# Kernel tuning notes

Measured on AMD Instinct MI355X. Metric: run time of the kernel, lower is better.

## Reference

```python
import jax, jax.numpy as jnp
import numpy as np

N = 100000        # nodes
E = 1600000       # directed edges (avg degree 16)
F_IN, F_HID, F_OUT = 512, 32, 16


def setup_inputs() -> dict:
    key = jax.random.key(0)
    k0, k1, k2, k3 = jax.random.split(key, 4)
    x = jax.random.normal(k0, (N, F_IN), dtype=jnp.float32)
    edge_index = jax.random.randint(k1, (2, E), 0, N, dtype=jnp.int32)
    # Glorot-ish init for the two GCNConv linear weights
    W1 = jax.random.normal(k2, (F_IN, F_HID), dtype=jnp.float32) / np.float32(np.sqrt(F_IN))
    W2 = jax.random.normal(k3, (F_HID, F_OUT), dtype=jnp.float32) / np.float32(np.sqrt(F_HID))
    b1 = jnp.zeros((F_HID,), jnp.float32)
    b2 = jnp.zeros((F_OUT,), jnp.float32)
    return {"x": x, "W1": W1, "b1": b1, "W2": W2, "b2": b2, "edge_index": edge_index}


def gcn_conv(x, W, b, src, dst):
    """PyG GCNConv: h = x W; symmetric-normalized aggregation with self-loops; + bias."""
    h = x @ W                                   # [N, F_out] project first (PyG order)
    # degree including the implicit self-loop (start from ones)
    deg = jnp.ones((N,), h.dtype).at[dst].add(1.0)
    dinv = jax.lax.rsqrt(deg)                   # deg^{-1/2}
    coef = (dinv[src] * dinv[dst])[:, None]     # [E, 1] edge norm
    msg = h[src] * coef                         # gather + scale
    agg = jax.ops.segment_sum(msg, dst, num_segments=N)  # scatter-add to dst
    agg = agg + h * (dinv * dinv)[:, None]      # self-loop contribution
    return agg + b


def reference(x, W1, b1, W2, b2, edge_index):
    src, dst = edge_index[0], edge_index[1]
    h = jax.nn.relu(gcn_conv(x, W1, b1, src, dst))
    # F.dropout(training=self.training) is identity in eval mode
    h = gcn_conv(h, W2, b2, src, dst)
    return jax.nn.log_softmax(h, axis=1)
```

## Files before the change

kernel.cpp:

```cpp
#include <hip/hip_runtime.h>
#include <hip/hip_bf16.h>
#include <cstdint>

#define NN   100000
#define NE   1600000
#define FIN  512
#define FHID 32
#define FOUT 16

#define BSHIFT 9
#define BSIZE  512
#define NBUCK  196
#define EPB    4096
#define NCHUNK ((NE + EPB - 1) / EPB)

typedef float f32x4 __attribute__((ext_vector_type(4)));
typedef short s16x8 __attribute__((ext_vector_type(8)));
typedef short s16x4 __attribute__((ext_vector_type(4)));
typedef unsigned int u32;
typedef unsigned short u16;

__device__ __forceinline__ short f2bf(float f) {
  union { float f; uint32_t u; } v; v.f = f;
  uint32_t r = v.u + 0x7fffu + ((v.u >> 16) & 1u);
  return (short)(r >> 16);
}
__device__ __forceinline__ float bf2f(u16 u) {
  union { uint32_t u; float f; } v; v.u = (uint32_t)u << 16; return v.f;
}

__global__ __launch_bounds__(256) void k_hist(const int* __restrict__ dst,
                                              u32* __restrict__ bcount) {
  __shared__ u32 h[NBUCK];
  int tid = threadIdx.x;
  if (tid < NBUCK) h[tid] = 0;
  __syncthreads();
  int base = blockIdx.x * EPB;
  #pragma unroll
  for (int i = 0; i < EPB / 256; ++i) {
    int e = base + i * 256 + tid;
    if (e < NE) atomicAdd(&h[dst[e] >> BSHIFT], 1u);
  }
  __syncthreads();
  if (tid < NBUCK && h[tid]) atomicAdd(&bcount[tid], h[tid]);
}

__global__ __launch_bounds__(256) void k_bscan(const u32* __restrict__ bc,
                                               u32* __restrict__ bstart,
                                               u32* __restrict__ bcur) {
  __shared__ u32 tmp[256];
  int tid = threadIdx.x;
  u32 v = (tid < NBUCK) ? bc[tid] : 0;
  tmp[tid] = v;
  __syncthreads();
  #pragma unroll
  for (int off = 1; off < 256; off <<= 1) {
    u32 t = (tid >= off) ? tmp[tid - off] : 0;
    __syncthreads();
    tmp[tid] += t;
    __syncthreads();
  }
  if (tid < NBUCK) { u32 e = tmp[tid] - v; bstart[tid] = e; bcur[tid] = e; }
  if (tid == 255) bstart[NBUCK] = tmp[255];
}

__global__ __launch_bounds__(256) void k_bin(const int* __restrict__ src,
                                             const int* __restrict__ dst,
                                             u32* __restrict__ bcur,
                                             u32* __restrict__ binned) {
  __shared__ u32 cnt[NBUCK];
  __shared__ u32 lofs[NBUCK];
  __shared__ u32 gbase[NBUCK];
  __shared__ u32 tmp[256];
  __shared__ u32 stage[EPB];
  __shared__ u16 sb[EPB];
  int tid = threadIdx.x;
  if (tid < NBUCK) cnt[tid] = 0;
  __syncthreads();

  int base = blockIdx.x * EPB;
  u32 vals[EPB / 256];
  u32 ofs[EPB / 256];
  int bks[EPB / 256];
  #pragma unroll
  for (int i = 0; i < EPB / 256; ++i) {
    int e = base + i * 256 + tid;
    bool ok = e < NE;
    int s = 0, d = 0;
    if (ok) { s = src[e]; d = dst[e]; }
    int b = ok ? (d >> BSHIFT) : -1;
    bks[i] = b;
    vals[i] = (u32)s | ((u32)(d & (BSIZE - 1)) << 17);
    ofs[i] = ok ? atomicAdd(&cnt[b], 1u) : 0;
  }
  __syncthreads();

  u32 cv = (tid < NBUCK) ? cnt[tid] : 0;
  tmp[tid] = cv;
  __syncthreads();
  #pragma unroll
  for (int off = 1; off < 256; off <<= 1) {
    u32 t = (tid >= off) ? tmp[tid - off] : 0;
    __syncthreads();
    tmp[tid] += t;
    __syncthreads();
  }
  if (tid < NBUCK) {
    lofs[tid] = tmp[tid] - cv;
    gbase[tid] = cv ? atomicAdd(&bcur[tid], cv) : 0;
  }
  __syncthreads();
  u32 total = tmp[255];
  __syncthreads();

  #pragma unroll
  for (int i = 0; i < EPB / 256; ++i) {
    if (bks[i] >= 0) {
      u32 sl = lofs[bks[i]] + ofs[i];
      stage[sl] = vals[i];
      sb[sl] = (u16)bks[i];
    }
  }
  __syncthreads();

  for (u32 s2 = tid; s2 < total; s2 += 256) {
    int b = sb[s2];
    binned[gbase[b] + (s2 - lofs[b])] = stage[s2];
  }
}

__global__ __launch_bounds__(256) void k_fin(const u32* __restrict__ binned,
                                             const u32* __restrict__ bstart,
                                             int* __restrict__ deg,
                                             int* __restrict__ rs,
                                             float* __restrict__ dinv,
                                             int* __restrict__ csr) {
  __shared__ u32 degl[BSIZE];
  __shared__ u32 rsl[BSIZE];
  __shared__ u32 tmp[256];
  int tid = threadIdx.x;
  int b = blockIdx.x;
  u32 start = bstart[b];
  u32 n = bstart[b + 1] - start;

  degl[tid] = 0; degl[tid + 256] = 0;
  __syncthreads();
  for (u32 k = tid; k < n; k += 256)
    atomicAdd(&degl[binned[start + k] >> 17], 1u);
  __syncthreads();

  u32 a0 = degl[2 * tid], a1 = degl[2 * tid + 1];
  u32 s = a0 + a1;
  tmp[tid] = s;
  __syncthreads();
  #pragma unroll
  for (int off = 1; off < 256; off <<= 1) {
    u32 t = (tid >= off) ? tmp[tid - off] : 0;
    __syncthreads();
    tmp[tid] += t;
    __syncthreads();
  }
  u32 e = tmp[tid] - s;
  rsl[2 * tid] = e;
  rsl[2 * tid + 1] = e + a0;
  __syncthreads();

  #pragma unroll
  for (int q = 0; q < 2; ++q) {
    int t = tid + q * 256;
    int g = b * BSIZE + t;
    if (g < NN) {
      deg[g] = (int)degl[t];
      rs[g] = (int)(start + rsl[t]);
      dinv[g] = rsqrtf(1.0f + (float)degl[t]);
    }
  }
  __syncthreads();

  for (u32 k = tid; k < n; k += 256) {
    u32 v = binned[start + k];
    u32 pos = atomicAdd(&rsl[v >> 17], 1u);
    csr[start + pos] = (int)(v & 0x1FFFFu);
  }
}

__global__ __launch_bounds__(256) void k_gemm1(const float* __restrict__ x,
                                               const float* __restrict__ W1,
                                               const float* __restrict__ dinv,
                                               u16* __restrict__ Hs1) {
  __shared__ s16x8 Blds[16][2][64];
  const int tid = threadIdx.x;
  for (int it = 0; it < 64; ++it) {
    int flat = it * 256 + tid;
    int i  = flat & 7;
    int l  = (flat >> 3) & 63;
    int nt = (flat >> 9) & 1;
    int kt = flat >> 10;
    int k  = kt * 32 + ((l >> 4) << 3) + i;
    int n  = nt * 16 + (l & 15);
    ((short*)Blds)[flat] = f2bf(W1[k * 32 + n]);
  }
  __syncthreads();

  const int lane = tid & 63;
  const int wv   = tid >> 6;
  const int h    = lane >> 4;
  const int m    = lane & 15;
  const int wid  = blockIdx.x * 4 + wv;
  if (wid >= 3125) return;
  const int t0 = wid * 2;

  const float* xr0 = x + (size_t)(t0 * 16 + m) * FIN + h * 8;
  const float* xr1 = xr0 + (size_t)16 * FIN;

  f32x4 acc[2][2] = {};
  #pragma unroll
  for (int kt = 0; kt < 16; ++kt) {
    f32x4 a0 = *(const f32x4*)(xr0 + kt * 32);
    f32x4 a1 = *(const f32x4*)(xr0 + kt * 32 + 4);
    f32x4 c0 = *(const f32x4*)(xr1 + kt * 32);
    f32x4 c1 = *(const f32x4*)(xr1 + kt * 32 + 4);
    s16x8 b0 = Blds[kt][0][lane];
    s16x8 b1 = Blds[kt][1][lane];
    s16x8 af, cf;
    af[0]=f2bf(a0[0]); af[1]=f2bf(a0[1]); af[2]=f2bf(a0[2]); af[3]=f2bf(a0[3]);
    af[4]=f2bf(a1[0]); af[5]=f2bf(a1[1]); af[6]=f2bf(a1[2]); af[7]=f2bf(a1[3]);
    cf[0]=f2bf(c0[0]); cf[1]=f2bf(c0[1]); cf[2]=f2bf(c0[2]); cf[3]=f2bf(c0[3]);
    cf[4]=f2bf(c1[0]); cf[5]=f2bf(c1[1]); cf[6]=f2bf(c1[2]); cf[7]=f2bf(c1[3]);
    acc[0][0] = __builtin_amdgcn_mfma_f32_16x16x32_bf16(af, b0, acc[0][0], 0, 0, 0);
    acc[0][1] = __builtin_amdgcn_mfma_f32_16x16x32_bf16(af, b1, acc[0][1], 0, 0, 0);
    acc[1][0] = __builtin_amdgcn_mfma_f32_16x16x32_bf16(cf, b0, acc[1][0], 0, 0, 0);
    acc[1][1] = __builtin_amdgcn_mfma_f32_16x16x32_bf16(cf, b1, acc[1][1], 0, 0, 0);
  }
  #pragma unroll
  for (int rt = 0; rt < 2; ++rt) {
    #pragma unroll
    for (int r = 0; r < 4; ++r) {
      int row = (t0 + rt) * 16 + h * 4 + r;
      float di = dinv[row];
      u16* o = Hs1 + (size_t)row * FHID + m;
      o[0]  = (u16)f2bf(acc[rt][0][r] * di);
      o[16] = (u16)f2bf(acc[rt][1][r] * di);
    }
  }
}

__global__ __launch_bounds__(256) void k_gat1(const int* __restrict__ csr,
                                              const int* __restrict__ rs,
                                              const int* __restrict__ deg,
                                              const float* __restrict__ dinv,
                                              const float* __restrict__ b1,
                                              const float* __restrict__ W2,
                                              const u16* __restrict__ Hs1,
                                              u16* __restrict__ Hs2) {
  __shared__ float w[FHID * FOUT];
  for (int i = threadIdx.x; i < FHID * FOUT; i += 256) w[i] = W2[i];
  __syncthreads();

  int t = blockIdx.x * 256 + threadIdx.x;
  int d = t >> 2;
  if (d >= NN) return;
  int p = t & 3;
  int start = rs[d], n = deg[d];

  float a0[8], a1[8], a2[8], a3[8];
  {
    s16x8 v = *(const s16x8*)(Hs1 + (size_t)d * FHID + p * 8);
    #pragma unroll
    for (int k = 0; k < 8; ++k) {
      a0[k] = bf2f((u16)v[k]); a1[k] = 0.f; a2[k] = 0.f; a3[k] = 0.f;
    }
  }
  int j = 0;
  for (; j + 4 <= n; j += 4) {
    int s0 = csr[start + j];
    int s1 = csr[start + j + 1];
    int s2 = csr[start + j + 2];
    int s3 = csr[start + j + 3];
    s16x8 v0 = *(const s16x8*)(Hs1 + (size_t)s0 * FHID + p * 8);
    s16x8 v1 = *(const s16x8*)(Hs1 + (size_t)s1 * FHID + p * 8);
    s16x8 v2 = *(const s16x8*)(Hs1 + (size_t)s2 * FHID + p * 8);
    s16x8 v3 = *(const s16x8*)(Hs1 + (size_t)s3 * FHID + p * 8);
    #pragma unroll
    for (int k = 0; k < 8; ++k) {
      a0[k] += bf2f((u16)v0[k]);
      a1[k] += bf2f((u16)v1[k]);
      a2[k] += bf2f((u16)v2[k]);
      a3[k] += bf2f((u16)v3[k]);
    }
  }
  for (; j < n; ++j) {
    int s0 = csr[start + j];
    s16x8 v0 = *(const s16x8*)(Hs1 + (size_t)s0 * FHID + p * 8);
    #pragma unroll
    for (int k = 0; k < 8; ++k) a0[k] += bf2f((u16)v0[k]);
  }

  float dd = dinv[d];
  float h[8];
  #pragma unroll
  for (int k = 0; k < 8; ++k)
    h[k] = fmaxf(((a0[k] + a1[k]) + (a2[k] + a3[k])) * dd + b1[p * 8 + k], 0.0f);

  float pj[FOUT];
  #pragma unroll
  for (int jj = 0; jj < FOUT; ++jj) pj[jj] = 0.f;
  #pragma unroll
  for (int k = 0; k < 8; ++k)
    #pragma unroll
    for (int jj = 0; jj < FOUT; ++jj)
      pj[jj] = fmaf(h[k], w[(p * 8 + k) * FOUT + jj], pj[jj]);
  #pragma unroll
  for (int jj = 0; jj < FOUT; ++jj) {
    pj[jj] += __shfl_xor(pj[jj], 1);
    pj[jj] += __shfl_xor(pj[jj], 2);
  }
  s16x4 o;
  #pragma unroll
  for (int q = 0; q < 4; ++q) o[q] = f2bf(pj[p * 4 + q] * dd);
  *(s16x4*)(Hs2 + (size_t)d * FOUT + p * 4) = o;
}

__global__ __launch_bounds__(256) void k_gat2(const int* __restrict__ csr,
                                              const int* __restrict__ rs,
                                              const int* __restrict__ deg,
                                              const float* __restrict__ dinv,
                                              const float* __restrict__ b2,
                                              const u16* __restrict__ Hs2,
                                              float* __restrict__ out) {
  int t = blockIdx.x * 256 + threadIdx.x;
  int d = t >> 1;
  if (d >= NN) return;
  int p = t & 1;
  int start = rs[d], n = deg[d];

  float a0[8], a1[8], a2[8], a3[8];
  {
    s16x8 v = *(const s16x8*)(Hs2 + (size_t)d * FOUT + p * 8);
    #pragma unroll
    for (int k = 0; k < 8; ++k) {
      a0[k] = bf2f((u16)v[k]); a1[k] = 0.f; a2[k] = 0.f; a3[k] = 0.f;
    }
  }
  int j = 0;
  for (; j + 4 <= n; j += 4) {
    int s0 = csr[start + j];
    int s1 = csr[start + j + 1];
    int s2 = csr[start + j + 2];
    int s3 = csr[start + j + 3];
    s16x8 v0 = *(const s16x8*)(Hs2 + (size_t)s0 * FOUT + p * 8);
    s16x8 v1 = *(const s16x8*)(Hs2 + (size_t)s1 * FOUT + p * 8);
    s16x8 v2 = *(const s16x8*)(Hs2 + (size_t)s2 * FOUT + p * 8);
    s16x8 v3 = *(const s16x8*)(Hs2 + (size_t)s3 * FOUT + p * 8);
    #pragma unroll
    for (int k = 0; k < 8; ++k) {
      a0[k] += bf2f((u16)v0[k]);
      a1[k] += bf2f((u16)v1[k]);
      a2[k] += bf2f((u16)v2[k]);
      a3[k] += bf2f((u16)v3[k]);
    }
  }
  for (; j < n; ++j) {
    int s0 = csr[start + j];
    s16x8 v0 = *(const s16x8*)(Hs2 + (size_t)s0 * FOUT + p * 8);
    #pragma unroll
    for (int k = 0; k < 8; ++k) a0[k] += bf2f((u16)v0[k]);
  }

  float dd = dinv[d];
  float z[8];
  #pragma unroll
  for (int k = 0; k < 8; ++k)
    z[k] = ((a0[k] + a1[k]) + (a2[k] + a3[k])) * dd + b2[p * 8 + k];

  float m = z[0];
  #pragma unroll
  for (int k = 1; k < 8; ++k) m = fmaxf(m, z[k]);
  m = fmaxf(m, __shfl_xor(m, 1));
  float s = 0.f;
  #pragma unroll
  for (int k = 0; k < 8; ++k) s += expf(z[k] - m);
  s += __shfl_xor(s, 1);
  float lse = m + logf(s);

  float* ob = out + (size_t)d * FOUT + p * 8;
  f32x4 o0 = { z[0]-lse, z[1]-lse, z[2]-lse, z[3]-lse };
  f32x4 o1 = { z[4]-lse, z[5]-lse, z[6]-lse, z[7]-lse };
  *(f32x4*)(ob)     = o0;
  *(f32x4*)(ob + 4) = o1;
}

extern "C" void kernel_launch(void* const* d_in, const int* in_sizes, int n_in,
                              void* d_out, int out_size, void* d_ws, size_t ws_size,
                              hipStream_t stream) {
  const float* x  = (const float*)d_in[0];
  const float* W1 = (const float*)d_in[1];
  const float* b1 = (const float*)d_in[2];
  const float* W2 = (const float*)d_in[3];
  const float* b2 = (const float*)d_in[4];
  const int*   ei = (const int*)d_in[5];
  const int* srcv = ei;
  const int* dstv = ei + NE;

  char* ws = (char*)d_ws;
  const size_t KB = 1024, MB = 1048576;
  u32*   bcount = (u32*)(ws + 0);
  u32*   bstart = (u32*)(ws + 4 * KB);
  u32*   bcur   = (u32*)(ws + 8 * KB);
  int*   deg    = (int*)(ws + 512 * KB);
  int*   rs     = (int*)(ws + 1024 * KB);
  float* dinv   = (float*)(ws + 1536 * KB);
  u32*   binned = (u32*)(ws + 2 * MB);
  int*   csr    = (int*)(ws + 9 * MB);
  u16*   Hs1    = (u16*)(ws + 16 * MB);
  u16*   Hs2    = (u16*)(ws + 23 * MB);
  float* out    = (float*)d_out;

  hipMemsetAsync(bcount, 0, NBUCK * sizeof(u32), stream);

  k_hist <<<NCHUNK, 256, 0, stream>>>(dstv, bcount);
  k_bscan<<<1,      256, 0, stream>>>(bcount, bstart, bcur);
  k_bin  <<<NCHUNK, 256, 0, stream>>>(srcv, dstv, bcur, binned);
  k_fin  <<<NBUCK,  256, 0, stream>>>(binned, bstart, deg, rs, dinv, csr);
  k_gemm1<<<782, 256, 0, stream>>>(x, W1, dinv, Hs1);
  k_gat1 <<<(NN * 4 + 255) / 256, 256, 0, stream>>>(csr, rs, deg, dinv, b1, W2, Hs1, Hs2);
  k_gat2 <<<(NN * 2 + 255) / 256, 256, 0, stream>>>(csr, rs, deg, dinv, b2, Hs2, out);
}
```

Before: 166.4 us.

## Halve bucket size, vectorize binning loads, unroll gathers, widen layer-2 threads

Bucket size drops from 512 to 256 nodes (391 buckets) and edges per chunk from 4096 to 2048. Binning and histogram kernels now load edges as int4 vectors with 512-thread blocks, and k_fin uses one thread per node. Both gather kernels get an 8-way unrolled neighbour loop to keep more independent loads in flight. Layer-2 aggregation moves to 4 threads per node with 4 features each, which doubles thread parallelism at the cost of narrower loads and more shuffles.

```diff
diff --git a/kernel.cpp b/kernel.cpp
--- a/kernel.cpp
+++ b/kernel.cpp
@@ -8,15 +8,16 @@
 #define FHID 32
 #define FOUT 16
 
-#define BSHIFT 9
-#define BSIZE  512
-#define NBUCK  196
-#define EPB    4096
+#define BSHIFT 8
+#define BSIZE  256
+#define NBUCK  391
+#define EPB    2048
 #define NCHUNK ((NE + EPB - 1) / EPB)
 
 typedef float f32x4 __attribute__((ext_vector_type(4)));
 typedef short s16x8 __attribute__((ext_vector_type(8)));
 typedef short s16x4 __attribute__((ext_vector_type(4)));
+typedef int   i32x4 __attribute__((ext_vector_type(4)));
 typedef unsigned int u32;
 typedef unsigned short u16;
 
@@ -33,65 +34,88 @@
                                               u32* __restrict__ bcount) {
   __shared__ u32 h[NBUCK];
   int tid = threadIdx.x;
-  if (tid < NBUCK) h[tid] = 0;
+  for (int i = tid; i < NBUCK; i += 256) h[i] = 0;
   __syncthreads();
   int base = blockIdx.x * EPB;
   #pragma unroll
-  for (int i = 0; i < EPB / 256; ++i) {
-    int e = base + i * 256 + tid;
-    if (e < NE) atomicAdd(&h[dst[e] >> BSHIFT], 1u);
-  }
-  __syncthreads();
-  if (tid < NBUCK && h[tid]) atomicAdd(&bcount[tid], h[tid]);
-}
-
-__global__ __launch_bounds__(256) void k_bscan(const u32* __restrict__ bc,
+  for (int i = 0; i < 2; ++i) {
+    int e0 = base + (i * 256 + tid) * 4;
+    if (e0 + 3 < NE) {
+      i32x4 d4 = *(const i32x4*)(dst + e0);
+      atomicAdd(&h[d4[0] >> BSHIFT], 1u);
+      atomicAdd(&h[d4[1] >> BSHIFT], 1u);
+      atomicAdd(&h[d4[2] >> BSHIFT], 1u);
+      atomicAdd(&h[d4[3] >> BSHIFT], 1u);
+    } else {
+      for (int k = 0; k < 4; ++k)
+        if (e0 + k < NE) atomicAdd(&h[dst[e0 + k] >> BSHIFT], 1u);
+    }
+  }
+  __syncthreads();
+  for (int i = tid; i < NBUCK; i += 256)
+    if (h[i]) atomicAdd(&bcount[i], h[i]);
+}
+
+__global__ __launch_bounds__(512) void k_bscan(const u32* __restrict__ bc,
                                                u32* __restrict__ bstart,
                                                u32* __restrict__ bcur) {
-  __shared__ u32 tmp[256];
+  __shared__ u32 tmp[512];
   int tid = threadIdx.x;
   u32 v = (tid < NBUCK) ? bc[tid] : 0;
   tmp[tid] = v;
   __syncthreads();
   #pragma unroll
-  for (int off = 1; off < 256; off <<= 1) {
+  for (int off = 1; off < 512; off <<= 1) {
     u32 t = (tid >= off) ? tmp[tid - off] : 0;
     __syncthreads();
     tmp[tid] += t;
     __syncthreads();
   }
   if (tid < NBUCK) { u32 e = tmp[tid] - v; bstart[tid] = e; bcur[tid] = e; }
-  if (tid == 255) bstart[NBUCK] = tmp[255];
-}
-
-__global__ __launch_bounds__(256) void k_bin(const int* __restrict__ src,
+  if (tid == 511) bstart[NBUCK] = tmp[511];
+}
+
+__global__ __launch_bounds__(512) void k_bin(const int* __restrict__ src,
                                              const int* __restrict__ dst,
                                              u32* __restrict__ bcur,
                                              u32* __restrict__ binned) {
   __shared__ u32 cnt[NBUCK];
   __shared__ u32 lofs[NBUCK];
   __shared__ u32 gbase[NBUCK];
-  __shared__ u32 tmp[256];
+  __shared__ u32 tmp[512];
   __shared__ u32 stage[EPB];
   __shared__ u16 sb[EPB];
   int tid = threadIdx.x;
-  if (tid < NBUCK) cnt[tid] = 0;
+  for (int i = tid; i < NBUCK; i += 512) cnt[i] = 0;
   __syncthreads();
 
   int base = blockIdx.x * EPB;
-  u32 vals[EPB / 256];
-  u32 ofs[EPB / 256];
-  int bks[EPB / 256];
-  #pragma unroll
-  for (int i = 0; i < EPB / 256; ++i) {
-    int e = base + i * 256 + tid;
-    bool ok = e < NE;
-    int s = 0, d = 0;
-    if (ok) { s = src[e]; d = dst[e]; }
-    int b = ok ? (d >> BSHIFT) : -1;
-    bks[i] = b;
-    vals[i] = (u32)s | ((u32)(d & (BSIZE - 1)) << 17);
-    ofs[i] = ok ? atomicAdd(&cnt[b], 1u) : 0;
+  int e0 = base + tid * 4;
+  u32 vals[4];
+  u32 ofs[4];
+  int bks[4];
+  if (e0 + 3 < NE) {
+    i32x4 s4 = *(const i32x4*)(src + e0);
+    i32x4 d4 = *(const i32x4*)(dst + e0);
+    #pragma unroll
+    for (int k = 0; k < 4; ++k) {
+      int b = d4[k] >> BSHIFT;
+      bks[k] = b;
+      vals[k] = (u32)s4[k] | ((u32)(d4[k] & (BSIZE - 1)) << 17);
+      ofs[k] = atomicAdd(&cnt[b], 1u);
+    }
+  } else {
+    #pragma unroll
+    for (int k = 0; k < 4; ++k) {
+      int e = e0 + k;
+      bool ok = e < NE;
+      int s = 0, d = 0;
+      if (ok) { s = src[e]; d = dst[e]; }
+      int b = ok ? (d >> BSHIFT) : -1;
+      bks[k] = b;
+      vals[k] = (u32)s | ((u32)(d & (BSIZE - 1)) << 17);
+      ofs[k] = ok ? atomicAdd(&cnt[b], 1u) : 0;
+    }
   }
   __syncthreads();
 
@@ -99,7 +123,7 @@
   tmp[tid] = cv;
   __syncthreads();
   #pragma unroll
-  for (int off = 1; off < 256; off <<= 1) {
+  for (int off = 1; off < 512; off <<= 1) {
     u32 t = (tid >= off) ? tmp[tid - off] : 0;
     __syncthreads();
     tmp[tid] += t;
@@ -110,20 +134,20 @@
     gbase[tid] = cv ? atomicAdd(&bcur[tid], cv) : 0;
   }
   __syncthreads();
-  u32 total = tmp[255];
-  __syncthreads();
-
-  #pragma unroll
-  for (int i = 0; i < EPB / 256; ++i) {
-    if (bks[i] >= 0) {
-      u32 sl = lofs[bks[i]] + ofs[i];
-      stage[sl] = vals[i];
-      sb[sl] = (u16)bks[i];
-    }
-  }
-  __syncthreads();
-
-  for (u32 s2 = tid; s2 < total; s2 += 256) {
+  u32 total = tmp[511];
+  __syncthreads();
+
+  #pragma unroll
+  for (int k = 0; k < 4; ++k) {
+    if (bks[k] >= 0) {
+      u32 sl = lofs[bks[k]] + ofs[k];
+      stage[sl] = vals[k];
+      sb[sl] = (u16)bks[k];
+    }
+  }
+  __syncthreads();
+
+  for (u32 s2 = tid; s2 < total; s2 += 512) {
     int b = sb[s2];
     binned[gbase[b] + (s2 - lofs[b])] = stage[s2];
   }
@@ -137,50 +161,43 @@
                                              int* __restrict__ csr) {
   __shared__ u32 degl[BSIZE];
   __shared__ u32 rsl[BSIZE];
-  __shared__ u32 tmp[256];
   int tid = threadIdx.x;
   int b = blockIdx.x;
   u32 start = bstart[b];
   u32 n = bstart[b + 1] - start;
 
-  degl[tid] = 0; degl[tid + 256] = 0;
+  degl[tid] = 0;
   __syncthreads();
   for (u32 k = tid; k < n; k += 256)
     atomicAdd(&degl[binned[start + k] >> 17], 1u);
   __syncthreads();
 
-  u32 a0 = degl[2 * tid], a1 = degl[2 * tid + 1];
-  u32 s = a0 + a1;
-  tmp[tid] = s;
+  u32 v = degl[tid];
+  rsl[tid] = v;
   __syncthreads();
   #pragma unroll
   for (int off = 1; off < 256; off <<= 1) {
-    u32 t = (tid >= off) ? tmp[tid - off] : 0;
-    __syncthreads();
-    tmp[tid] += t;
-    __syncthreads();
-  }
-  u32 e = tmp[tid] - s;
-  rsl[2 * tid] = e;
-  rsl[2 * tid + 1] = e + a0;
-  __syncthreads();
-
-  #pragma unroll
-  for (int q = 0; q < 2; ++q) {
-    int t = tid + q * 256;
-    int g = b * BSIZE + t;
-    if (g < NN) {
-      deg[g] = (int)degl[t];
-      rs[g] = (int)(start + rsl[t]);
-      dinv[g] = rsqrtf(1.0f + (float)degl[t]);
-    }
+    u32 t = (tid >= off) ? rsl[tid - off] : 0;
+    __syncthreads();
+    rsl[tid] += t;
+    __syncthreads();
+  }
+  u32 e = rsl[tid] - v;
+  __syncthreads();
+  rsl[tid] = e;
+
+  int g = b * BSIZE + tid;
+  if (g < NN) {
+    deg[g] = (int)v;
+    rs[g] = (int)(start + e);
+    dinv[g] = rsqrtf(1.0f + (float)v);
   }
   __syncthreads();
 
   for (u32 k = tid; k < n; k += 256) {
-    u32 v = binned[start + k];
-    u32 pos = atomicAdd(&rsl[v >> 17], 1u);
-    csr[start + pos] = (int)(v & 0x1FFFFu);
+    u32 vv = binned[start + k];
+    u32 pos = atomicAdd(&rsl[vv >> 17], 1u);
+    csr[start + pos] = (int)(vv & 0x1FFFFu);
   }
 }
 
@@ -272,6 +289,35 @@
     }
   }
   int j = 0;
+  for (; j + 8 <= n; j += 8) {
+    int s0 = csr[start + j];
+    int s1 = csr[start + j + 1];
+    int s2 = csr[start + j + 2];
+    int s3 = csr[start + j + 3];
+    int s4 = csr[start + j + 4];
+    int s5 = csr[start + j + 5];
+    int s6 = csr[start + j + 6];
+    int s7 = csr[start + j + 7];
+    s16x8 v0 = *(const s16x8*)(Hs1 + (size_t)s0 * FHID + p * 8);
+    s16x8 v1 = *(const s16x8*)(Hs1 + (size_t)s1 * FHID + p * 8);
+    s16x8 v2 = *(const s16x8*)(Hs1 + (size_t)s2 * FHID + p * 8);
+    s16x8 v3 = *(const s16x8*)(Hs1 + (size_t)s3 * FHID + p * 8);
+    s16x8 v4 = *(const s16x8*)(Hs1 + (size_t)s4 * FHID + p * 8);
+    s16x8 v5 = *(const s16x8*)(Hs1 + (size_t)s5 * FHID + p * 8);
+    s16x8 v6 = *(const s16x8*)(Hs1 + (size_t)s6 * FHID + p * 8);
+    s16x8 v7 = *(const s16x8*)(Hs1 + (size_t)s7 * FHID + p * 8);
+    #pragma unroll
+    for (int k = 0; k < 8; ++k) {
+      a0[k] += bf2f((u16)v0[k]);
+      a1[k] += bf2f((u16)v1[k]);
+      a2[k] += bf2f((u16)v2[k]);
+      a3[k] += bf2f((u16)v3[k]);
+      a0[k] += bf2f((u16)v4[k]);
+      a1[k] += bf2f((u16)v5[k]);
+      a2[k] += bf2f((u16)v6[k]);
+      a3[k] += bf2f((u16)v7[k]);
+    }
+  }
   for (; j + 4 <= n; j += 4) {
     int s0 = csr[start + j];
     int s1 = csr[start + j + 1];
@@ -329,65 +375,89 @@
                                               const u16* __restrict__ Hs2,
                                               float* __restrict__ out) {
   int t = blockIdx.x * 256 + threadIdx.x;
-  int d = t >> 1;
+  int d = t >> 2;
   if (d >= NN) return;
-  int p = t & 1;
+  int p = t & 3;
   int start = rs[d], n = deg[d];
 
-  float a0[8], a1[8], a2[8], a3[8];
+  float a0[4], a1[4], a2[4], a3[4];
   {
-    s16x8 v = *(const s16x8*)(Hs2 + (size_t)d * FOUT + p * 8);
-    #pragma unroll
-    for (int k = 0; k < 8; ++k) {
+    s16x4 v = *(const s16x4*)(Hs2 + (size_t)d * FOUT + p * 4);
+    #pragma unroll
+    for (int k = 0; k < 4; ++k) {
       a0[k] = bf2f((u16)v[k]); a1[k] = 0.f; a2[k] = 0.f; a3[k] = 0.f;
     }
   }
   int j = 0;
-  for (; j + 4 <= n; j += 4) {
+  for (; j + 8 <= n; j += 8) {
     int s0 = csr[start + j];
     int s1 = csr[start + j + 1];
     int s2 = csr[start + j + 2];
     int s3 = csr[start + j + 3];
-    s16x8 v0 = *(const s16x8*)(Hs2 + (size_t)s0 * FOUT + p * 8);
-    s16x8 v1 = *(const s16x8*)(Hs2 + (size_t)s1 * FOUT + p * 8);
-    s16x8 v2 = *(const s16x8*)(Hs2 + (size_t)s2 * FOUT + p * 8);
-    s16x8 v3 = *(const s16x8*)(Hs2 + (size_t)s3 * FOUT + p * 8);
-    #pragma unroll
-    for (int k = 0; k < 8; ++k) {
+    int s4 = csr[start + j + 4];
+    int s5 = csr[start + j + 5];
+    int s6 = csr[start + j + 6];
+    int s7 = csr[start + j + 7];
+    s16x4 v0 = *(const s16x4*)(Hs2 + (size_t)s0 * FOUT + p * 4);
+    s16x4 v1 = *(const s16x4*)(Hs2 + (size_t)s1 * FOUT + p * 4);
+    s16x4 v2 = *(const s16x4*)(Hs2 + (size_t)s2 * FOUT + p * 4);
+    s16x4 v3 = *(const s16x4*)(Hs2 + (size_t)s3 * FOUT + p * 4);
+    s16x4 v4 = *(const s16x4*)(Hs2 + (size_t)s4 * FOUT + p * 4);
+    s16x4 v5 = *(const s16x4*)(Hs2 + (size_t)s5 * FOUT + p * 4);
+    s16x4 v6 = *(const s16x4*)(Hs2 + (size_t)s6 * FOUT + p * 4);
+    s16x4 v7 = *(const s16x4*)(Hs2 + (size_t)s7 * FOUT + p * 4);
+    #pragma unroll
+    for (int k = 0; k < 4; ++k) {
       a0[k] += bf2f((u16)v0[k]);
       a1[k] += bf2f((u16)v1[k]);
       a2[k] += bf2f((u16)v2[k]);
       a3[k] += bf2f((u16)v3[k]);
+      a0[k] += bf2f((u16)v4[k]);
+      a1[k] += bf2f((u16)v5[k]);
+      a2[k] += bf2f((u16)v6[k]);
+      a3[k] += bf2f((u16)v7[k]);
+    }
+  }
+  for (; j + 4 <= n; j += 4) {
+    int s0 = csr[start + j];
+    int s1 = csr[start + j + 1];
+    int s2 = csr[start + j + 2];
+    int s3 = csr[start + j + 3];
+    s16x4 v0 = *(const s16x4*)(Hs2 + (size_t)s0 * FOUT + p * 4);
+    s16x4 v1 = *(const s16x4*)(Hs2 + (size_t)s1 * FOUT + p * 4);
+    s16x4 v2 = *(const s16x4*)(Hs2 + (size_t)s2 * FOUT + p * 4);
+    s16x4 v3 = *(const s16x4*)(Hs2 + (size_t)s3 * FOUT + p * 4);
+    #pragma unroll
+    for (int k = 0; k < 4; ++k) {
+      a0[k] += bf2f((u16)v0[k]);
+      a1[k] += bf2f((u16)v1[k]);
+      a2[k] += bf2f((u16)v2[k]);
+      a3[k] += bf2f((u16)v3[k]);
     }
   }
   for (; j < n; ++j) {
     int s0 = csr[start + j];
-    s16x8 v0 = *(const s16x8*)(Hs2 + (size_t)s0 * FOUT + p * 8);
-    #pragma unroll
-    for (int k = 0; k < 8; ++k) a0[k] += bf2f((u16)v0[k]);
+    s16x4 v0 = *(const s16x4*)(Hs2 + (size_t)s0 * FOUT + p * 4);
+    #pragma unroll
+    for (int k = 0; k < 4; ++k) a0[k] += bf2f((u16)v0[k]);
   }
 
   float dd = dinv[d];
-  float z[8];
-  #pragma unroll
-  for (int k = 0; k < 8; ++k)
-    z[k] = ((a0[k] + a1[k]) + (a2[k] + a3[k])) * dd + b2[p * 8 + k];
-
-  float m = z[0];
-  #pragma unroll
-  for (int k = 1; k < 8; ++k) m = fmaxf(m, z[k]);
+  float z[4];
+  #pragma unroll
+  for (int k = 0; k < 4; ++k)
+    z[k] = ((a0[k] + a1[k]) + (a2[k] + a3[k])) * dd + b2[p * 4 + k];
+
+  float m = fmaxf(fmaxf(z[0], z[1]), fmaxf(z[2], z[3]));
   m = fmaxf(m, __shfl_xor(m, 1));
-  float s = 0.f;
-  #pragma unroll
-  for (int k = 0; k < 8; ++k) s += expf(z[k] - m);
+  m = fmaxf(m, __shfl_xor(m, 2));
+  float s = expf(z[0]-m) + expf(z[1]-m) + expf(z[2]-m) + expf(z[3]-m);
   s += __shfl_xor(s, 1);
+  s += __shfl_xor(s, 2);
   float lse = m + logf(s);
 
-  float* ob = out + (size_t)d * FOUT + p * 8;
-  f32x4 o0 = { z[0]-lse, z[1]-lse, z[2]-lse, z[3]-lse };
-  f32x4 o1 = { z[4]-lse, z[5]-lse, z[6]-lse, z[7]-lse };
-  *(f32x4*)(ob)     = o0;
-  *(f32x4*)(ob + 4) = o1;
+  f32x4 o = { z[0]-lse, z[1]-lse, z[2]-lse, z[3]-lse };
+  *(f32x4*)(out + (size_t)d * FOUT + p * 4) = o;
 }
 
 extern "C" void kernel_launch(void* const* d_in, const int* in_sizes, int n_in,
@@ -405,8 +475,8 @@
   char* ws = (char*)d_ws;
   const size_t KB = 1024, MB = 1048576;
   u32*   bcount = (u32*)(ws + 0);
-  u32*   bstart = (u32*)(ws + 4 * KB);
-  u32*   bcur   = (u32*)(ws + 8 * KB);
+  u32*   bstart = (u32*)(ws + 8 * KB);
+  u32*   bcur   = (u32*)(ws + 16 * KB);
   int*   deg    = (int*)(ws + 512 * KB);
   int*   rs     = (int*)(ws + 1024 * KB);
   float* dinv   = (float*)(ws + 1536 * KB);
@@ -419,10 +489,10 @@
   hipMemsetAsync(bcount, 0, NBUCK * sizeof(u32), stream);
 
   k_hist <<<NCHUNK, 256, 0, stream>>>(dstv, bcount);
-  k_bscan<<<1,      256, 0, stream>>>(bcount, bstart, bcur);
-  k_bin  <<<NCHUNK, 256, 0, stream>>>(srcv, dstv, bcur, binned);
+  k_bscan<<<1,      512, 0, stream>>>(bcount, bstart, bcur);
+  k_bin  <<<NCHUNK, 512, 0, stream>>>(srcv, dstv, bcur, binned);
   k_fin  <<<NBUCK,  256, 0, stream>>>(binned, bstart, deg, rs, dinv, csr);
   k_gemm1<<<782, 256, 0, stream>>>(x, W1, dinv, Hs1);
   k_gat1 <<<(NN * 4 + 255) / 256, 256, 0, stream>>>(csr, rs, deg, dinv, b1, W2, Hs1, Hs2);
-  k_gat2 <<<(NN * 2 + 255) / 256, 256, 0, stream>>>(csr, rs, deg, dinv, b2, Hs2, out);
-}
+  k_gat2 <<<(NN * 4 + 255) / 256, 256, 0, stream>>>(csr, rs, deg, dinv, b2, Hs2, out);
+}
```

Result: no change. 164.3 us (-1.3%).
